# Optimization experiments

Measured on AMD Instinct MI355X. Metric: run time of the kernel, lower is better.

Reference implementation:

```python
import jax, jax.numpy as jnp
import numpy as np

B, T, XD, ZD, H = 1024, 1000, 8, 8, 256


def setup_inputs() -> dict:
    key = jax.random.key(0)
    ks = jax.random.split(key, 10)
    # monotonically increasing time grid, identical per batch element: [B, T, 1]
    t = jnp.broadcast_to(jnp.linspace(0.0, 10.0, T, dtype=jnp.float32)[None, :, None], (B, T, 1))
    x = jax.random.normal(ks[0], (B, T, XD), jnp.float32)
    z = jax.random.normal(ks[1], (B, T, ZD), jnp.float32)
    event_t = jax.random.uniform(ks[2], (B, 1), jnp.float32, 3.0, 7.0)
    z_jump = jax.random.normal(ks[3], (B, ZD), jnp.float32)
    in_dim = 3 * (XD + ZD)

    def lin(k, fan_in, fan_out):
        return jax.random.normal(k, (fan_in, fan_out), jnp.float32) * (1.0 / np.sqrt(fan_in))

    W1 = lin(ks[4], in_dim, H); b1 = jnp.zeros((H,), jnp.float32)
    W2 = lin(ks[5], H, H);     b2 = jnp.zeros((H,), jnp.float32)
    W3 = lin(ks[6], H, H);     b3 = jnp.zeros((H,), jnp.float32)
    W4 = lin(ks[7], H, XD);    b4 = jnp.zeros((XD,), jnp.float32)
    return dict(t=t, x=x, z=z, event_t=event_t, z_jump=z_jump,
                W1=W1, b1=b1, W2=W2, b2=b2, W3=W3, b3=b3, W4=W4, b4=b4)


def reference(t, x, z, event_t, z_jump, W1, b1, W2, b2, W3, b3, W4, b4):
    # all_initial = cat(x[:,0], z[:,0]) : [B, XD+ZD]
    all_initial = jnp.concatenate([x[:, 0], z[:, 0]], axis=-1)

    def de_func(x_cur, z_eff):
        xtzt = jnp.concatenate([x_cur, z_eff], axis=-1)                      # [B, XD+ZD]
        inp = jnp.concatenate([all_initial, xtzt - all_initial, xtzt], -1)   # [B, 3*(XD+ZD)]
        h = jax.nn.elu(inp @ W1 + b1)
        h = jax.nn.elu(h @ W2 + b2)
        h = jax.nn.elu(h @ W3 + b3)
        return h @ W4 + b4                                                   # [B, XD]

    t_seq = jnp.moveaxis(t, 1, 0)   # [T, B, 1]
    z_seq = jnp.moveaxis(z, 1, 0)   # [T, B, ZD]
    dt = t_seq[1:] - t_seq[:-1]     # [T-1, B, 1]

    def step(x_cur, step_in):
        t_i, dt_i, z_i = step_in
        # event: once t passes event_t, exogenous z jumps to z_jump
        z_eff = jnp.where(t_i >= event_t, z_jump, z_i)
        x_next = x_cur + dt_i * de_func(x_cur, z_eff)  # explicit Euler step
        return x_next, x_next

    x0 = x[:, 0]  # initial condition [B, XD]
    _, xs = jax.lax.scan(step, x0, (t_seq[:-1], dt, z_seq[:-1]))
    sol = jnp.concatenate([x0[None], xs], axis=0)  # [T, B, XD]
    return jnp.moveaxis(sol, 0, 1)                 # [B, T, XD]
```

## Files before the change

kernel.cpp:

```cpp
#include <hip/hip_runtime.h>
#include <cstdint>
#include <cstddef>

typedef __bf16 bf16x8 __attribute__((ext_vector_type(8)));
typedef float f32x4 __attribute__((ext_vector_type(4)));

#define HD 256
#define TLEN 1000
#define NSTEP 999
#define BTILE 4

#define W1F_OFF 0
#define W1C_OFF 8192
#define W2R_OFF 16384
#define W3R_OFF 81920
#define W4R_OFF 147456
#define WS_ELEMS 151552

__device__ __forceinline__ void wg_barrier() {
  asm volatile("s_waitcnt lgkmcnt(0)\n\ts_barrier" ::: "memory");
}

__global__ void prep_weights(const float* __restrict__ W1, const float* __restrict__ b1,
                             const float* __restrict__ W2, const float* __restrict__ W3,
                             const float* __restrict__ W4, __bf16* __restrict__ ws) {
  int tid = blockIdx.x * blockDim.x + threadIdx.x;
  if (tid >= WS_ELEMS) return;
  float val = 0.0f;
  if (tid < W1C_OFF) {
    int t = tid;
    int j = t & 7, lane = (t >> 3) & 63, tt = (t >> 9) & 1, w = (t >> 10) & 7;
    int k = ((lane >> 4) * 8) + j;
    int n = w * 32 + tt * 16 + (lane & 15);
    if (k < 8) val = W1[(16 + k) * HD + n] + W1[(32 + k) * HD + n];
    else if (k < 16) { int d = k - 8; val = W1[(24 + d) * HD + n] + W1[(40 + d) * HD + n]; }
  } else if (tid < W2R_OFF) {
    int t = tid - W1C_OFF;
    int j = t & 7, lane = (t >> 3) & 63, tt = (t >> 9) & 1, w = (t >> 10) & 7;
    int k = ((lane >> 4) * 8) + j;
    int n = w * 32 + tt * 16 + (lane & 15);
    if (k < 8) val = W1[k * HD + n] - W1[(16 + k) * HD + n];
    else if (k < 16) { int d = k - 8; val = W1[(8 + d) * HD + n] - W1[(24 + d) * HD + n]; }
    else if (k == 16) val = b1[n];
  } else if (tid < W3R_OFF) {
    int t = tid - W2R_OFF;
    int j = t & 7, lane = (t >> 3) & 63, tt = (t >> 9) & 1, kb = (t >> 10) & 7, w = (t >> 13) & 7;
    int k = kb * 32 + ((lane >> 4) * 8) + j;
    int n = w * 32 + tt * 16 + (lane & 15);
    val = W2[k * HD + n];
  } else if (tid < W4R_OFF) {
    int t = tid - W3R_OFF;
    int j = t & 7, lane = (t >> 3) & 63, tt = (t >> 9) & 1, kb = (t >> 10) & 7, w = (t >> 13) & 7;
    int k = kb * 32 + ((lane >> 4) * 8) + j;
    int n = w * 32 + tt * 16 + (lane & 15);
    val = W3[k * HD + n];
  } else {
    int t = tid - W4R_OFF;
    int j = t & 7, lane = (t >> 3) & 63, kb = (t >> 9) & 7;
    int k = kb * 32 + ((lane >> 4) * 8) + j;
    int n = lane & 15;
    val = (n < 8) ? W4[k * 8 + n] : 0.0f;
  }
  ws[tid] = (__bf16)val;
}

__global__ __launch_bounds__(512, 2) void ode_main(
    const float* __restrict__ t_g, const float* __restrict__ x_g,
    const float* __restrict__ z_g, const float* __restrict__ ev_g,
    const float* __restrict__ zj_g, const float* __restrict__ b2_g,
    const float* __restrict__ b3_g, const float* __restrict__ b4_g,
    const __bf16* __restrict__ ws, float* __restrict__ out) {
  __shared__ __align__(16) __bf16 h_a[16 * 264];
  __shared__ __align__(16) __bf16 h_b[16 * 264];
  __shared__ __align__(16) float p4[8 * 16 * 8];
  __shared__ __align__(16) float x_cur[16 * 12];
  __shared__ __align__(16) float z_eff[16 * 12];
  __shared__ __align__(16) float x0s[16 * 12];
  __shared__ __align__(16) float z0s[16 * 12];
  __shared__ __align__(16) float zjs[16 * 12];
  __shared__ float evs[16];

  const int tid  = threadIdx.x;
  const int lane = tid & 63;
  const int wid  = tid >> 6;
  const int bcol = lane & 15;
  const int q    = lane >> 4;
  const int b0   = blockIdx.x * BTILE;
  const bool live = bcol < BTILE;

  if (tid < 128) {
    int m = tid >> 3, d = tid & 7;
    if (m < BTILE) {
      size_t gb = (size_t)(b0 + m);
      float x0 = x_g[gb * (TLEN * 8) + d];
      float z0 = z_g[gb * (TLEN * 8) + d];
      x0s[m * 12 + d] = x0;
      z0s[m * 12 + d] = z0;
      x_cur[m * 12 + d] = x0;
      zjs[m * 12 + d] = zj_g[gb * 8 + d];
      out[gb * (TLEN * 8) + d] = x0;
      if (d == 0) evs[m] = ev_g[gb];
    } else {
      x0s[m * 12 + d] = 0.f;
      z0s[m * 12 + d] = 0.f;
      x_cur[m * 12 + d] = 0.f;
      zjs[m * 12 + d] = 0.f;
      if (d == 0) evs[m] = 0.f;
    }
  }
  __syncthreads();

  if (tid < 128) {
    int m = tid >> 3, d = tid & 7;
    float t0 = t_g[0];
    z_eff[m * 12 + d] = (t0 >= evs[m]) ? zjs[m * 12 + d] : z0s[m * 12 + d];
  }

  const bf16x8* wsv = (const bf16x8*)ws;
  bf16x8 w1ff[2], w2f[8][2], w3f[8][2];
#pragma unroll
  for (int tt = 0; tt < 2; ++tt)
    w1ff[tt] = wsv[(W1F_OFF / 8) + (wid * 2 + tt) * 64 + lane];
#pragma unroll
  for (int kb = 0; kb < 8; ++kb)
#pragma unroll
    for (int tt = 0; tt < 2; ++tt) {
      w2f[kb][tt] = wsv[(W2R_OFF / 8) + ((wid * 8 + kb) * 2 + tt) * 64 + lane];
      w3f[kb][tt] = wsv[(W3R_OFF / 8) + ((wid * 8 + kb) * 2 + tt) * 64 + lane];
    }
  bf16x8 w4f = wsv[(W4R_OFF / 8) + wid * 64 + lane];

  f32x4 b2v[2], b3v[2];
#pragma unroll
  for (int tt = 0; tt < 2; ++tt) {
    int n0 = wid * 32 + tt * 16 + q * 4;
    b2v[tt] = *(const f32x4*)(b2_g + n0);
    b3v[tt] = *(const f32x4*)(b3_g + n0);
  }
  float b4l = (tid < 64) ? b4_g[tid & 7] : 0.0f;

  const int m1 = lane >> 2;
  const int d0 = (lane & 3) * 2;
  float2 zjf = make_float2(0.f, 0.f);
  float ev1 = 0.f;
  const bool zprod = (wid == 2) && (lane < BTILE * 4);
  if (zprod) {
    zjf.x = zjs[m1 * 12 + d0];
    zjf.y = zjs[m1 * 12 + d0 + 1];
    ev1 = evs[m1];
  }

  bf16x8 zf;
#pragma unroll
  for (int e = 0; e < 8; ++e) zf[e] = (__bf16)0.f;

  f32x4 c1init[2];
  {
    bf16x8 cfrag = zf;
    if (q == 0) {
      const float* xp = x0s + bcol * 12;
#pragma unroll
      for (int e = 0; e < 4; ++e) { cfrag[e] = (__bf16)xp[e]; cfrag[e + 4] = (__bf16)xp[e + 4]; }
    } else if (q == 1) {
      const float* zp = z0s + bcol * 12;
#pragma unroll
      for (int e = 0; e < 4; ++e) { cfrag[e] = (__bf16)zp[e]; cfrag[e + 4] = (__bf16)zp[e + 4]; }
    } else if (q == 2) {
      cfrag[0] = (__bf16)1.0f;
    }
    f32x4 z4 = {0.f, 0.f, 0.f, 0.f};
#pragma unroll
    for (int tt = 0; tt < 2; ++tt) {
      bf16x8 w1cf = wsv[(W1C_OFF / 8) + (wid * 2 + tt) * 64 + lane];
      c1init[tt] = __builtin_amdgcn_mfma_f32_16x16x32_bf16(w1cf, cfrag, z4, 0, 0, 0);
    }
  }

  __syncthreads();

  float tc = t_g[0];

  bf16x8 bfr[8];
#pragma unroll
  for (int kb = 0; kb < 8; ++kb) bfr[kb] = zf;
  bf16x8 h4r = zf;

  auto layer = [&](const __bf16* src, __bf16* dst, const bf16x8 (*wf)[2], const f32x4* bv) {
    const bf16x8* hp = (const bf16x8*)src;
    if (live) {
#pragma unroll
      for (int kb = 0; kb < 8; ++kb) bfr[kb] = hp[bcol * 33 + kb * 4 + q];
    }
#pragma unroll
    for (int tt = 0; tt < 2; ++tt) {
      f32x4 c = bv[tt];
#pragma unroll
      for (int kb = 0; kb < 8; ++kb)
        c = __builtin_amdgcn_mfma_f32_16x16x32_bf16(wf[kb][tt], bfr[kb], c, 0, 0, 0);
      union { __bf16 h4[4]; unsigned long long u; } pk;
#pragma unroll
      for (int e = 0; e < 4; ++e) {
        float v = c[e];
        v = (v > 0.f) ? v : (__expf(v) - 1.0f);
        pk.h4[e] = (__bf16)v;
      }
      if (live)
        *(unsigned long long*)(dst + bcol * 264 + wid * 32 + tt * 16 + q * 4) = pk.u;
    }
  };

#pragma unroll 1
  for (int i = 0; i < NSTEP; ++i) {
    float tn = t_g[i + 1];
    float2 zpre = make_float2(0.f, 0.f);
    if (zprod)
      zpre = *(const float2*)(z_g + ((size_t)(b0 + m1) * TLEN + (i + 1)) * 8 + d0);

    {
      bf16x8 f = zf;
      if (q < 2) {
        const float* rp = ((q & 1) ? z_eff : x_cur) + bcol * 12;
        f32x4 r0 = *(const f32x4*)(rp);
        f32x4 r1 = *(const f32x4*)(rp + 4);
#pragma unroll
        for (int e = 0; e < 4; ++e) { f[e] = (__bf16)r0[e]; f[e + 4] = (__bf16)r1[e]; }
      }
#pragma unroll
      for (int tt = 0; tt < 2; ++tt) {
        f32x4 c = __builtin_amdgcn_mfma_f32_16x16x32_bf16(w1ff[tt], f, c1init[tt], 0, 0, 0);
        union { __bf16 h4[4]; unsigned long long u; } pk;
#pragma unroll
        for (int e = 0; e < 4; ++e) {
          float v = c[e];
          v = (v > 0.f) ? v : (__expf(v) - 1.0f);
          pk.h4[e] = (__bf16)v;
        }
        if (live)
          *(unsigned long long*)(h_a + bcol * 264 + wid * 32 + tt * 16 + q * 4) = pk.u;
      }
    }
    wg_barrier();
    layer(h_a, h_b, w2f, b2v);
    wg_barrier();
    layer(h_b, h_a, w3f, b3v);

    {
      const bf16x8* hp = (const bf16x8*)h_a;
      if (live) h4r = hp[bcol * 33 + wid * 4 + q];
      f32x4 c = {0.f, 0.f, 0.f, 0.f};
      c = __builtin_amdgcn_mfma_f32_16x16x32_bf16(w4f, h4r, c, 0, 0, 0);
      if (q < 2 && live)
        *(f32x4*)(p4 + wid * 128 + bcol * 8 + q * 4) = c;
    }
    wg_barrier();

    float dt = tn - tc;
    if (tid < 64) {
      int m = tid >> 3, d = tid & 7;
      if (m < BTILE) {
        float s = b4l;
#pragma unroll
        for (int j = 0; j < 8; ++j) s += p4[j * 128 + m * 8 + d];
        float xn = x_cur[m * 12 + d] + dt * s;
        x_cur[m * 12 + d] = xn;
        out[(size_t)(b0 + m) * (TLEN * 8) + (size_t)(i + 1) * 8 + d] = xn;
      }
    } else if (zprod) {
      bool jmp = (tn >= ev1);
      float2 zev = make_float2(jmp ? zjf.x : zpre.x, jmp ? zjf.y : zpre.y);
      *(float2*)(z_eff + m1 * 12 + d0) = zev;
    }
    tc = tn;
    wg_barrier();
  }
}

extern "C" void kernel_launch(void* const* d_in, const int* in_sizes, int n_in,
                              void* d_out, int out_size, void* d_ws, size_t ws_size,
                              hipStream_t stream) {
  const float* t  = (const float*)d_in[0];
  const float* x  = (const float*)d_in[1];
  const float* z  = (const float*)d_in[2];
  const float* ev = (const float*)d_in[3];
  const float* zj = (const float*)d_in[4];
  const float* W1 = (const float*)d_in[5];
  const float* b1 = (const float*)d_in[6];
  const float* W2 = (const float*)d_in[7];
  const float* b2 = (const float*)d_in[8];
  const float* W3 = (const float*)d_in[9];
  const float* b3 = (const float*)d_in[10];
  const float* W4 = (const float*)d_in[11];
  const float* b4 = (const float*)d_in[12];
  __bf16* ws = (__bf16*)d_ws;
  float* out = (float*)d_out;

  prep_weights<<<592, 256, 0, stream>>>(W1, b1, W2, W3, W4, ws);
  ode_main<<<256, 512, 0, stream>>>(t, x, z, ev, zj, b2, b3, b4, ws, out);
}
```

Measured before the change: 1.591 ms.

## Keep Euler state in registers redundantly per wave to drop a barrier per step

Each wave now reduces the layer-4 partial sums itself and keeps the Euler state x in registers, with wave 0 writing the output. This removes the shared x_cur buffer and one of the four workgroup barriers per time step. The z_eff update is moved between the layer-1 and layer-2 barriers, and the reduction loop is reordered to run at the start of the next iteration. The cost is redundant reduction work in all eight waves and unconditional LDS reads for dead columns.

```diff
diff --git a/kernel.cpp b/kernel.cpp
--- a/kernel.cpp
+++ b/kernel.cpp
@@ -72,8 +72,7 @@
     const __bf16* __restrict__ ws, float* __restrict__ out) {
   __shared__ __align__(16) __bf16 h_a[16 * 264];
   __shared__ __align__(16) __bf16 h_b[16 * 264];
-  __shared__ __align__(16) float p4[8 * 16 * 8];
-  __shared__ __align__(16) float x_cur[16 * 12];
+  __shared__ __align__(16) float p4[8 * 128];
   __shared__ __align__(16) float z_eff[16 * 12];
   __shared__ __align__(16) float x0s[16 * 12];
   __shared__ __align__(16) float z0s[16 * 12];
@@ -87,27 +86,25 @@
   const int q    = lane >> 4;
   const int b0   = blockIdx.x * BTILE;
   const bool live = bcol < BTILE;
+  const int rrow = live ? bcol : 0;
+  const size_t gb = (size_t)(b0 + (live ? bcol : 0));
 
   if (tid < 128) {
     int m = tid >> 3, d = tid & 7;
     if (m < BTILE) {
-      size_t gb = (size_t)(b0 + m);
-      float x0 = x_g[gb * (TLEN * 8) + d];
-      float z0 = z_g[gb * (TLEN * 8) + d];
-      x0s[m * 12 + d] = x0;
-      z0s[m * 12 + d] = z0;
-      x_cur[m * 12 + d] = x0;
-      zjs[m * 12 + d] = zj_g[gb * 8 + d];
-      out[gb * (TLEN * 8) + d] = x0;
-      if (d == 0) evs[m] = ev_g[gb];
+      size_t g = (size_t)(b0 + m);
+      x0s[m * 12 + d] = x_g[g * (TLEN * 8) + d];
+      z0s[m * 12 + d] = z_g[g * (TLEN * 8) + d];
+      zjs[m * 12 + d] = zj_g[g * 8 + d];
+      if (d == 0) evs[m] = ev_g[g];
     } else {
       x0s[m * 12 + d] = 0.f;
       z0s[m * 12 + d] = 0.f;
-      x_cur[m * 12 + d] = 0.f;
       zjs[m * 12 + d] = 0.f;
       if (d == 0) evs[m] = 0.f;
     }
   }
+  if (tid < 512) { p4[tid] = 0.f; p4[tid + 512] = 0.f; }
   __syncthreads();
 
   if (tid < 128) {
@@ -137,7 +134,8 @@
     b2v[tt] = *(const f32x4*)(b2_g + n0);
     b3v[tt] = *(const f32x4*)(b3_g + n0);
   }
-  float b4l = (tid < 64) ? b4_g[tid & 7] : 0.0f;
+  f32x4 b4v = {0.f, 0.f, 0.f, 0.f};
+  if (q < 2) b4v = *(const f32x4*)(b4_g + q * 4);
 
   const int m1 = lane >> 2;
   const int d0 = (lane & 3) * 2;
@@ -176,21 +174,19 @@
     }
   }
 
+  f32x4 x4 = {0.f, 0.f, 0.f, 0.f};
+  if (q < 2) x4 = *(const f32x4*)(x0s + bcol * 12 + q * 4);
+
   __syncthreads();
 
   float tc = t_g[0];
-
-  bf16x8 bfr[8];
-#pragma unroll
-  for (int kb = 0; kb < 8; ++kb) bfr[kb] = zf;
-  bf16x8 h4r = zf;
+  float tn_hold = tc;
 
   auto layer = [&](const __bf16* src, __bf16* dst, const bf16x8 (*wf)[2], const f32x4* bv) {
     const bf16x8* hp = (const bf16x8*)src;
-    if (live) {
-#pragma unroll
-      for (int kb = 0; kb < 8; ++kb) bfr[kb] = hp[bcol * 33 + kb * 4 + q];
-    }
+    bf16x8 bfr[8];
+#pragma unroll
+    for (int kb = 0; kb < 8; ++kb) bfr[kb] = hp[rrow * 33 + kb * 4 + q];
 #pragma unroll
     for (int tt = 0; tt < 2; ++tt) {
       f32x4 c = bv[tt];
@@ -210,67 +206,74 @@
   };
 
 #pragma unroll 1
-  for (int i = 0; i < NSTEP; ++i) {
-    float tn = t_g[i + 1];
+  for (int i = 0; i <= NSTEP; ++i) {
+    float tn = tn_hold;
+    float dt = tn - tc;
+    tc = tn;
+    if (q < 2 && live) {
+      const float* pp = p4 + bcol * 8 + q * 4;
+      f32x4 s = {0.f, 0.f, 0.f, 0.f};
+#pragma unroll
+      for (int j = 0; j < 8; ++j) s += *(const f32x4*)(pp + j * 128);
+#pragma unroll
+      for (int e = 0; e < 4; ++e) x4[e] += dt * (s[e] + b4v[e]);
+      if (wid == 0)
+        *(f32x4*)(out + gb * (TLEN * 8) + (size_t)i * 8 + q * 4) = x4;
+    }
+    if (i == NSTEP) break;
+
     float2 zpre = make_float2(0.f, 0.f);
     if (zprod)
       zpre = *(const float2*)(z_g + ((size_t)(b0 + m1) * TLEN + (i + 1)) * 8 + d0);
 
-    {
-      bf16x8 f = zf;
-      if (q < 2) {
-        const float* rp = ((q & 1) ? z_eff : x_cur) + bcol * 12;
-        f32x4 r0 = *(const f32x4*)(rp);
-        f32x4 r1 = *(const f32x4*)(rp + 4);
-#pragma unroll
-        for (int e = 0; e < 4; ++e) { f[e] = (__bf16)r0[e]; f[e + 4] = (__bf16)r1[e]; }
+    f32x4 xo;
+#pragma unroll
+    for (int e = 0; e < 4; ++e) xo[e] = __shfl_xor(x4[e], 16);
+    bf16x8 f = zf;
+    if (q == 0) {
+#pragma unroll
+      for (int e = 0; e < 4; ++e) { f[e] = (__bf16)x4[e]; f[e + 4] = (__bf16)xo[e]; }
+    } else if (q == 1) {
+      const float* rp = z_eff + bcol * 12;
+      f32x4 r0 = *(const f32x4*)(rp);
+      f32x4 r1 = *(const f32x4*)(rp + 4);
+#pragma unroll
+      for (int e = 0; e < 4; ++e) { f[e] = (__bf16)r0[e]; f[e + 4] = (__bf16)r1[e]; }
+    }
+#pragma unroll
+    for (int tt = 0; tt < 2; ++tt) {
+      f32x4 c = __builtin_amdgcn_mfma_f32_16x16x32_bf16(w1ff[tt], f, c1init[tt], 0, 0, 0);
+      union { __bf16 h4[4]; unsigned long long u; } pk;
+#pragma unroll
+      for (int e = 0; e < 4; ++e) {
+        float v = c[e];
+        v = (v > 0.f) ? v : (__expf(v) - 1.0f);
+        pk.h4[e] = (__bf16)v;
       }
-#pragma unroll
-      for (int tt = 0; tt < 2; ++tt) {
-        f32x4 c = __builtin_amdgcn_mfma_f32_16x16x32_bf16(w1ff[tt], f, c1init[tt], 0, 0, 0);
-        union { __bf16 h4[4]; unsigned long long u; } pk;
-#pragma unroll
-        for (int e = 0; e < 4; ++e) {
-          float v = c[e];
-          v = (v > 0.f) ? v : (__expf(v) - 1.0f);
-          pk.h4[e] = (__bf16)v;
-        }
-        if (live)
-          *(unsigned long long*)(h_a + bcol * 264 + wid * 32 + tt * 16 + q * 4) = pk.u;
-      }
+      if (live)
+        *(unsigned long long*)(h_a + bcol * 264 + wid * 32 + tt * 16 + q * 4) = pk.u;
     }
     wg_barrier();
+
+    if (zprod) {
+      tn_hold = t_g[i + 1];
+      bool jmp = (tn_hold >= ev1);
+      float2 zev = make_float2(jmp ? zjf.x : zpre.x, jmp ? zjf.y : zpre.y);
+      *(float2*)(z_eff + m1 * 12 + d0) = zev;
+    } else {
+      tn_hold = t_g[i + 1];
+    }
     layer(h_a, h_b, w2f, b2v);
     wg_barrier();
+
     layer(h_b, h_a, w3f, b3v);
-
     {
-      const bf16x8* hp = (const bf16x8*)h_a;
-      if (live) h4r = hp[bcol * 33 + wid * 4 + q];
+      bf16x8 h4r = ((const bf16x8*)h_a)[rrow * 33 + wid * 4 + q];
       f32x4 c = {0.f, 0.f, 0.f, 0.f};
       c = __builtin_amdgcn_mfma_f32_16x16x32_bf16(w4f, h4r, c, 0, 0, 0);
       if (q < 2 && live)
         *(f32x4*)(p4 + wid * 128 + bcol * 8 + q * 4) = c;
     }
-    wg_barrier();
-
-    float dt = tn - tc;
-    if (tid < 64) {
-      int m = tid >> 3, d = tid & 7;
-      if (m < BTILE) {
-        float s = b4l;
-#pragma unroll
-        for (int j = 0; j < 8; ++j) s += p4[j * 128 + m * 8 + d];
-        float xn = x_cur[m * 12 + d] + dt * s;
-        x_cur[m * 12 + d] = xn;
-        out[(size_t)(b0 + m) * (TLEN * 8) + (size_t)(i + 1) * 8 + d] = xn;
-      }
-    } else if (zprod) {
-      bool jmp = (tn >= ev1);
-      float2 zev = make_float2(jmp ? zjf.x : zpre.x, jmp ? zjf.y : zpre.y);
-      *(float2*)(z_eff + m1 * 12 + d0) = zev;
-    }
-    tc = tn;
     wg_barrier();
   }
 }
```

Result: slower. 1.874 ms (+17.8%).
